# Kernel tuning notes

Measured on AMD Instinct MI355X. Metric: run time of the kernel, lower is better.

The kernel has to match this reference:

```python
import jax, jax.numpy as jnp
import numpy as np

N_NODES = 50000
N_EDGES = 600000
N_GRAPHS = 2048
EMB = 128
N_LAYERS = 3
ATOM_FEATS, ATOM_VOCAB = 9, 100
BOND_FEATS, BOND_VOCAB, BOND_DIM = 3, 8, 3


def setup_inputs() -> dict:
    key = jax.random.key(0)
    ks = jax.random.split(key, 10)
    x = jax.random.randint(ks[0], (N_NODES, ATOM_FEATS), 0, ATOM_VOCAB)
    edge_index = jax.random.randint(ks[1], (2, N_EDGES), 0, N_NODES)
    edge_attr = jax.random.randint(ks[2], (N_EDGES, BOND_FEATS), 0, BOND_VOCAB)
    batch = jnp.sort(jax.random.randint(ks[3], (N_NODES,), 0, N_GRAPHS))
    s = 1.0 / np.sqrt(EMB).astype(np.float32)
    atom_emb = jax.random.normal(ks[4], (ATOM_FEATS, ATOM_VOCAB, EMB), jnp.float32) * 0.1
    bond_emb = jax.random.normal(ks[5], (N_LAYERS, BOND_FEATS, BOND_VOCAB, BOND_DIM), jnp.float32) * 0.1
    W = jax.random.normal(ks[6], (N_LAYERS, BOND_DIM, EMB, EMB), jnp.float32) * s
    b = jnp.zeros((N_LAYERS, BOND_DIM, EMB), jnp.float32)
    fc1_w = jax.random.normal(ks[7], (EMB, EMB), jnp.float32) * s
    fc1_b = jnp.zeros((EMB,), jnp.float32)
    fc2_w = jax.random.normal(ks[8], (EMB, 1), jnp.float32) * s
    fc2_b = jnp.zeros((1,), jnp.float32)
    return dict(x=x, edge_index=edge_index, edge_attr=edge_attr, batch=batch,
                atom_emb=atom_emb, bond_emb=bond_emb, W=W, b=b,
                fc1_w=fc1_w, fc1_b=fc1_b, fc2_w=fc2_w, fc2_b=fc2_b)


def reference(x, edge_index, edge_attr, batch, atom_emb, bond_emb, W, b,
              fc1_w, fc1_b, fc2_w, fc2_b):
    src, dst = edge_index[0], edge_index[1]
    n = x.shape[0]
    # AtomEncoder: sum of per-column embedding lookups -> [N, EMB]
    h = atom_emb[0][x[:, 0]]
    for c in range(1, ATOM_FEATS):
        h = h + atom_emb[c][x[:, c]]
    for layer in range(N_LAYERS):
        # BondEncoder: [E, BOND_DIM] edge weights (one scalar channel per conv)
        ew = bond_emb[layer, 0][edge_attr[:, 0]]
        for c in range(1, BOND_FEATS):
            ew = ew + bond_emb[layer, c][edge_attr[:, c]]
        # Three parallel GCNConv(normalize=False): linear, gather src, edge-weight, scatter-add to dst
        msg = jnp.zeros((edge_index.shape[1], EMB), h.dtype)
        for k in range(BOND_DIM):
            xw = h @ W[layer, k]              # [N, EMB]
            msg = msg + ew[:, k:k + 1] * xw[src]   # [E, EMB]
        agg = jax.ops.segment_sum(msg, dst, num_segments=n)
        hn = agg + jnp.sum(b[layer], axis=0)  # sum of the three conv biases
        if layer < N_LAYERS - 1:
            hn = jax.nn.relu(hn)              # dropout is identity at eval
        h = hn + h                            # residual
    # global_mean_pool
    sums = jax.ops.segment_sum(h, batch, num_segments=N_GRAPHS)
    counts = jax.ops.segment_sum(jnp.ones((n,), h.dtype), batch, num_segments=N_GRAPHS)
    hg = sums / jnp.maximum(counts, 1.0)[:, None]
    return (hg @ fc1_w + fc1_b) @ fc2_w + fc2_b   # [N_GRAPHS, 1]
```

## Files before the change

kernel.cpp:

```cpp
#include <hip/hip_runtime.h>

#define N_NODES 50000
#define N_EDGES 600000
#define N_GRAPHS 2048
#define EMB 128
#define TDIM 384
#define TS_LD 392
#define HN (N_NODES * EMB)
#define GROWS 64

#define EPB 2048
#define NBLKA ((N_EDGES + EPB - 1) / EPB)
#define NCOARSE ((N_NODES + 255) / 256)

#define PRE_ATOM_NB 8334
#define PRE_WCONV_NB 384
#define PRE_GB_NB 131

typedef __attribute__((ext_vector_type(8))) short bf16x8;
typedef __attribute__((ext_vector_type(4))) float f32x4;
#define MFMA_BF16(a, b, c) __builtin_amdgcn_mfma_f32_16x16x32_bf16(a, b, c, 0, 0, 0)

#define AS1 __attribute__((address_space(1)))
#define AS3 __attribute__((address_space(3)))
__device__ inline void gl_lds16(const void* g, void* l) {
  __builtin_amdgcn_global_load_lds((const AS1 void*)g, (AS3 void*)l, 16, 0, 0);
}

__device__ inline unsigned short f2bf(float f) {
  unsigned int u = __float_as_uint(f);
  u += 0x7fffu + ((u >> 16) & 1u);
  return (unsigned short)(u >> 16);
}
__device__ inline float bf2f(unsigned short b) {
  return __uint_as_float(((unsigned int)b) << 16);
}
__device__ inline bf16x8 pack8(float4 lo, float4 hi) {
  bf16x8 r;
  r[0] = (short)f2bf(lo.x); r[1] = (short)f2bf(lo.y);
  r[2] = (short)f2bf(lo.z); r[3] = (short)f2bf(lo.w);
  r[4] = (short)f2bf(hi.x); r[5] = (short)f2bf(hi.y);
  r[6] = (short)f2bf(hi.z); r[7] = (short)f2bf(hi.w);
  return r;
}

__global__ __launch_bounds__(384) void k_pre(const int* __restrict__ x,
                                             const float* __restrict__ atom_emb,
                                             unsigned short* __restrict__ h_bf,
                                             const float* __restrict__ W,
                                             unsigned short* __restrict__ wt,
                                             const int* __restrict__ batch,
                                             int* __restrict__ gs) {
  __shared__ float sb[6 * 1280];
  int blk = blockIdx.x;
  if (blk < PRE_ATOM_NB) {
    const int wv = threadIdx.x >> 6;
    const int lane = threadIdx.x & 63;
    int n = blk * 6 + wv;
    if (n < N_NODES) {
      const int nu = __builtin_amdgcn_readfirstlane(n);
      const int* xr = x + nu * 9;
      int ix[9];
#pragma unroll
      for (int c = 0; c < 9; ++c) ix[c] = xr[c];
      float* wbase = sb + wv * 1280;
      const int half = lane >> 5;
      const int sub16 = lane & 31;
#pragma unroll
      for (int j = 0; j < 4; ++j) {
        int c = 2 * j + half;
        const float* g = atom_emb + (size_t)(c * 100 + ix[c]) * EMB + sub16 * 4;
        gl_lds16(g, wbase + j * 256);
      }
      {
        const float* g = atom_emb + (size_t)(8 * 100 + ix[8]) * EMB + sub16 * 4;
        gl_lds16(g, wbase + 1024);
      }
      asm volatile("s_waitcnt vmcnt(0)" ::: "memory");
      float2 acc = {0.f, 0.f};
#pragma unroll
      for (int c = 0; c < 9; ++c) {
        float2 v = *(const float2*)(wbase + c * 128 + lane * 2);
        acc.x += v.x; acc.y += v.y;
      }
      *(ushort2*)(h_bf + (size_t)nu * EMB + lane * 2) = ushort2{f2bf(acc.x), f2bf(acc.y)};
    }
    return;
  }
  blk -= PRE_ATOM_NB;
  if (blk < PRE_WCONV_NB) {
    int layer = blk >> 7, c = blk & 127, k = threadIdx.x;
    float v = W[(((layer * 3 + (k >> 7)) * 128) + (k & 127)) * 128 + c];
    wt[(size_t)blk * 384 + k] = f2bf(v);
    return;
  }
  blk -= PRE_WCONV_NB;
  {
    int i = blk * 384 + threadIdx.x;
    if (i < N_NODES) {
      int b = batch[i];
      int bp = (i == 0) ? -1 : batch[i - 1];
      for (int g = bp + 1; g <= b; ++g) gs[g] = i;
      if (i == N_NODES - 1) {
        for (int g = b + 1; g <= N_GRAPHS; ++g) gs[g] = N_NODES;
      }
    }
  }
}

__global__ __launch_bounds__(256) void k_cnt(const int* __restrict__ ei,
                                             int* __restrict__ ghist) {
  __shared__ int h[256];
  const int t = threadIdx.x;
  h[t] = 0;
  __syncthreads();
  const int base = blockIdx.x * EPB;
#pragma unroll
  for (int k = 0; k < 8; ++k) {
    int e = base + k * 256 + t;
    if (e < N_EDGES) atomicAdd(&h[ei[N_EDGES + e] >> 8], 1);
  }
  __syncthreads();
  if (t < NCOARSE) ghist[(size_t)t * NBLKA + blockIdx.x] = h[t];
}

__global__ __launch_bounds__(256) void k_sscan(int* __restrict__ ghist,
                                               int* __restrict__ bucket_base,
                                               int* __restrict__ row_start) {
  __shared__ int s[256];
  const int t = threadIdx.x;
  int sum = 0;
  if (t < NCOARSE) {
    int* row = ghist + (size_t)t * NBLKA;
    for (int b = 0; b < NBLKA; ++b) { int v = row[b]; row[b] = sum; sum += v; }
  }
  s[t] = sum;
  __syncthreads();
  for (int off = 1; off < 256; off <<= 1) {
    int v = (t >= off) ? s[t - off] : 0;
    __syncthreads();
    s[t] += v;
    __syncthreads();
  }
  if (t < NCOARSE) bucket_base[t] = s[t] - sum;
  if (t == 0) { bucket_base[NCOARSE] = N_EDGES; row_start[N_NODES] = N_EDGES; }
}

__global__ __launch_bounds__(256) void k_coarse(const int* __restrict__ ei,
                                                const int* __restrict__ ea,
                                                const int* __restrict__ ghist,
                                                const int* __restrict__ bucket_base,
                                                int2* __restrict__ tmp) {
  __shared__ int cnt[256];
  const int t = threadIdx.x;
  cnt[t] = 0;
  __syncthreads();
  const int base = blockIdx.x * EPB;
#pragma unroll
  for (int k = 0; k < 8; ++k) {
    int e = base + k * 256 + t;
    if (e < N_EDGES) {
      int dst = ei[N_EDGES + e];
      int d = dst >> 8;
      int r = atomicAdd(&cnt[d], 1);
      int pos = bucket_base[d] + ghist[(size_t)d * NBLKA + blockIdx.x] + r;
      int eap = ea[e * 3 + 0] | (ea[e * 3 + 1] << 3) | (ea[e * 3 + 2] << 6);
      tmp[pos] = int2{dst | (eap << 16), ei[e]};
    }
  }
}

__global__ __launch_bounds__(256) void k_fine(const int2* __restrict__ tmp,
                                              const int* __restrict__ bucket_base,
                                              int* __restrict__ row_start,
                                              int2* __restrict__ sorted_se) {
  __shared__ int h[256];
  __shared__ int s[256];
  __shared__ int ex[256];
  const int t = threadIdx.x;
  const int d = blockIdx.x;
  const int b0 = bucket_base[d], b1 = bucket_base[d + 1];
  h[t] = 0;
  __syncthreads();
  for (int i = b0 + t; i < b1; i += 256) atomicAdd(&h[tmp[i].x & 255], 1);
  __syncthreads();
  s[t] = h[t];
  __syncthreads();
  for (int off = 1; off < 256; off <<= 1) {
    int v = (t >= off) ? s[t - off] : 0;
    __syncthreads();
    s[t] += v;
    __syncthreads();
  }
  ex[t] = s[t] - h[t];
  int node = d * 256 + t;
  if (node < N_NODES) row_start[node] = b0 + ex[t];
  h[t] = 0;
  __syncthreads();
  for (int i = b0 + t; i < b1; i += 256) {
    int2 r = tmp[i];
    int f = r.x & 255;
    int pos = b0 + ex[f] + atomicAdd(&h[f], 1);
    sorted_se[pos] = int2{r.y, (r.x >> 16) & 511};
  }
}

__global__ __launch_bounds__(256) void k_agg(const int2* __restrict__ sorted_se,
                                             const int* __restrict__ row_start,
                                             const float* __restrict__ bl,
                                             const unsigned short* __restrict__ h_bf,
                                             unsigned short* __restrict__ t_bf) {
  __shared__ float4 combo[512];
  for (int c = threadIdx.x; c < 512; c += 256) {
    int a0 = c & 7, a1 = (c >> 3) & 7, a2 = (c >> 6) & 7;
    combo[c] = float4{bl[a0 * 3 + 0] + bl[24 + a1 * 3 + 0] + bl[48 + a2 * 3 + 0],
                      bl[a0 * 3 + 1] + bl[24 + a1 * 3 + 1] + bl[48 + a2 * 3 + 1],
                      bl[a0 * 3 + 2] + bl[24 + a1 * 3 + 2] + bl[48 + a2 * 3 + 2], 0.f};
  }
  __syncthreads();
  const int node = blockIdx.x * 16 + (threadIdx.x >> 4);
  const int sub = threadIdx.x & 15;
  const int beg = row_start[node], end = row_start[node + 1];
  float4 l0 = {0.f, 0.f, 0.f, 0.f}, h0 = l0;
  float4 l1 = l0, h1 = l0;
  float4 l2 = l0, h2 = l0;
  int e = beg;
  const int full_end = beg + ((end - beg) & ~7);
  for (; e < full_end; e += 8) {
    int2 se[8];
#pragma unroll
    for (int j = 0; j < 8; ++j) se[j] = sorted_se[e + j];
    bf16x8 u[8];
#pragma unroll
    for (int j = 0; j < 8; ++j)
      u[j] = *(const bf16x8*)(h_bf + (size_t)se[j].x * EMB + sub * 8);
#pragma unroll
    for (int j = 0; j < 8; ++j) {
      float4 w = combo[se[j].y];
      float4 vlo = {bf2f((unsigned short)u[j][0]), bf2f((unsigned short)u[j][1]),
                    bf2f((unsigned short)u[j][2]), bf2f((unsigned short)u[j][3])};
      float4 vhi = {bf2f((unsigned short)u[j][4]), bf2f((unsigned short)u[j][5]),
                    bf2f((unsigned short)u[j][6]), bf2f((unsigned short)u[j][7])};
      l0 += vlo * w.x; h0 += vhi * w.x;
      l1 += vlo * w.y; h1 += vhi * w.y;
      l2 += vlo * w.z; h2 += vhi * w.z;
    }
  }
  if (e < end) {
    int2 se[8];
#pragma unroll
    for (int j = 0; j < 8; ++j) {
      int idx = e + j;
      se[j] = sorted_se[idx < end ? idx : end - 1];
    }
    bf16x8 u[8];
#pragma unroll
    for (int j = 0; j < 8; ++j)
      u[j] = *(const bf16x8*)(h_bf + (size_t)se[j].x * EMB + sub * 8);
#pragma unroll
    for (int j = 0; j < 8; ++j) {
      float4 w = (e + j < end) ? combo[se[j].y] : float4{0.f, 0.f, 0.f, 0.f};
      float4 vlo = {bf2f((unsigned short)u[j][0]), bf2f((unsigned short)u[j][1]),
                    bf2f((unsigned short)u[j][2]), bf2f((unsigned short)u[j][3])};
      float4 vhi = {bf2f((unsigned short)u[j][4]), bf2f((unsigned short)u[j][5]),
                    bf2f((unsigned short)u[j][6]), bf2f((unsigned short)u[j][7])};
      l0 += vlo * w.x; h0 += vhi * w.x;
      l1 += vlo * w.y; h1 += vhi * w.y;
      l2 += vlo * w.z; h2 += vhi * w.z;
    }
  }
  size_t base = (size_t)node * TDIM + sub * 8;
  *(bf16x8*)(t_bf + base)       = pack8(l0, h0);
  *(bf16x8*)(t_bf + base + 128) = pack8(l1, h1);
  *(bf16x8*)(t_bf + base + 256) = pack8(l2, h2);
}

__global__ __launch_bounds__(512) void k_gemm(const unsigned short* __restrict__ t_bf,
                                              const unsigned short* __restrict__ wt,
                                              const float* __restrict__ bl,
                                              const unsigned short* __restrict__ h_in_bf,
                                              unsigned short* __restrict__ h_out_bf,
                                              int do_relu) {
  __shared__ unsigned short ts[GROWS * TS_LD];
  const int nb = blockIdx.x * GROWS;
  for (int i = threadIdx.x; i < GROWS * 48; i += 512) {
    int r = i / 48, cc = i % 48;
    bf16x8 v = {};
    int row = nb + r;
    if (row < N_NODES) v = *(const bf16x8*)(t_bf + (size_t)row * TDIM + cc * 8);
    *(bf16x8*)(ts + r * TS_LD + cc * 8) = v;
  }
  __syncthreads();

  const int wv = threadIdx.x >> 6;
  const int lane = threadIdx.x & 63;
  const int m = lane & 15;
  const int kq = lane >> 4;
  const int c = wv * 16 + m;

  const unsigned short* pB = wt + (size_t)c * TDIM + kq * 8;
  bf16x8 B[12];
#pragma unroll
  for (int kc = 0; kc < 12; ++kc) B[kc] = *(const bf16x8*)(pB + kc * 32);

  const float bias = bl[c] + bl[128 + c] + bl[256 + c];

#pragma unroll
  for (int rt = 0; rt < 4; ++rt) {
    const unsigned short* pA = ts + (rt * 16 + m) * TS_LD + kq * 8;
    bf16x8 A[12];
#pragma unroll
    for (int kc = 0; kc < 12; ++kc) A[kc] = *(const bf16x8*)(pA + kc * 32);
    f32x4 acc = {0.f, 0.f, 0.f, 0.f};
#pragma unroll
    for (int kc = 0; kc < 12; ++kc) acc = MFMA_BF16(A[kc], B[kc], acc);
#pragma unroll
    for (int r = 0; r < 4; ++r) {
      int row = nb + rt * 16 + kq * 4 + r;
      if (row < N_NODES) {
        size_t idx = (size_t)row * EMB + c;
        float v = acc[r] + bias;
        if (do_relu) v = fmaxf(v, 0.f);
        float hn = bf2f(h_in_bf[idx]) + v;
        h_out_bf[idx] = f2bf(hn);
      }
    }
  }
}

__global__ __launch_bounds__(128) void k_head(const unsigned short* __restrict__ h_bf,
                                              const int* __restrict__ gs,
                                              const float* __restrict__ fc1_w,
                                              const float* __restrict__ fc1_b,
                                              const float* __restrict__ fc2_w,
                                              const float* __restrict__ fc2_b,
                                              float* __restrict__ out) {
  __shared__ float hg[EMB];
  __shared__ float red[EMB];
  int g = blockIdx.x, e = threadIdx.x;
  int ns = gs[g], ne = gs[g + 1];
  float acc = 0.f;
  for (int n = ns; n < ne; ++n) acc += bf2f(h_bf[(size_t)n * EMB + e]);
  float cnt = fmaxf((float)(ne - ns), 1.f);
  hg[e] = acc / cnt;
  __syncthreads();
  float a2 = fc1_b[e];
  for (int j = 0; j < EMB; ++j) a2 += hg[j] * fc1_w[j * EMB + e];
  red[e] = a2 * fc2_w[e];
  __syncthreads();
  for (int s = 64; s > 0; s >>= 1) {
    if (e < s) red[e] += red[e + s];
    __syncthreads();
  }
  if (e == 0) out[g] = red[0] + fc2_b[0];
}

extern "C" void kernel_launch(void* const* d_in, const int* in_sizes, int n_in,
                              void* d_out, int out_size, void* d_ws, size_t ws_size,
                              hipStream_t stream) {
  const int*   x        = (const int*)d_in[0];
  const int*   ei       = (const int*)d_in[1];
  const int*   ea       = (const int*)d_in[2];
  const int*   batch    = (const int*)d_in[3];
  const float* atom_emb = (const float*)d_in[4];
  const float* bond_emb = (const float*)d_in[5];
  const float* W        = (const float*)d_in[6];
  const float* b        = (const float*)d_in[7];
  const float* fc1_w    = (const float*)d_in[8];
  const float* fc1_b    = (const float*)d_in[9];
  const float* fc2_w    = (const float*)d_in[10];
  const float* fc2_b    = (const float*)d_in[11];
  float* out = (float*)d_out;

  char* p = (char*)d_ws;
  auto alloc = [&](size_t bytes) { char* r = p; p += (bytes + 255) & ~(size_t)255; return r; };
  unsigned short* h0_bf      = (unsigned short*)alloc((size_t)HN * 2);
  unsigned short* h1_bf      = (unsigned short*)alloc((size_t)HN * 2);
  unsigned short* t_bf       = (unsigned short*)alloc((size_t)N_NODES * TDIM * 2);
  unsigned short* wt         = (unsigned short*)alloc((size_t)3 * 128 * TDIM * 2);
  int*            gs         = (int*)alloc((size_t)(N_GRAPHS + 1) * 4);
  int*            row_start  = (int*)alloc((size_t)(N_NODES + 1) * 4);
  int*            ghist      = (int*)alloc((size_t)NCOARSE * NBLKA * 4);
  int*            bucket_base= (int*)alloc((size_t)(NCOARSE + 1) * 4);
  int2*           tmp_se     = (int2*)alloc((size_t)N_EDGES * 8);
  int2*           sorted_se  = (int2*)alloc((size_t)(N_EDGES + 8) * 8);

  const int pre_blocks = PRE_ATOM_NB + PRE_WCONV_NB + PRE_GB_NB;
  k_pre<<<pre_blocks, 384, 0, stream>>>(x, atom_emb, h0_bf, W, wt, batch, gs);
  k_cnt<<<NBLKA, 256, 0, stream>>>(ei, ghist);
  k_sscan<<<1, 256, 0, stream>>>(ghist, bucket_base, row_start);
  k_coarse<<<NBLKA, 256, 0, stream>>>(ei, ea, ghist, bucket_base, tmp_se);
  k_fine<<<NCOARSE, 256, 0, stream>>>(tmp_se, bucket_base, row_start, sorted_se);

  unsigned short* hib = h0_bf;
  unsigned short* hob = h1_bf;
  const int gemm_blocks = (N_NODES + GROWS - 1) / GROWS;
  for (int layer = 0; layer < 3; ++layer) {
    k_agg<<<N_NODES / 16, 256, 0, stream>>>(sorted_se, row_start, bond_emb + layer * 72,
                                            hib, t_bf);
    k_gemm<<<gemm_blocks, 512, 0, stream>>>(
        t_bf, wt + (size_t)layer * 128 * TDIM, b + layer * 3 * EMB,
        hib, hob, layer < 2 ? 1 : 0);
    unsigned short* tb = hib; hib = hob; hob = tb;
  }

  k_head<<<N_GRAPHS, 128, 0, stream>>>(hib, gs, fc1_w, fc1_b, fc2_w, fc2_b, out);
}
```

Measured before the change: 358.3 us.

## Replace single-block serial histogram scan with three-pass multi-block global scan

The old single-block scan had each of 196 threads serially walk its row of 293 histogram entries, with strided global memory access, and then did a small block scan. The new version flattens the bucket-major histogram into one exclusive scan spread across many blocks: block-local scans, a one-block scan of the block partials, and an add-back pass that also writes the bucket bases. k_coarse then reads absolute offsets directly. This adds two kernel launches in exchange for removing the long serial, uncoalesced loop.

```diff
diff --git a/kernel.cpp b/kernel.cpp
--- a/kernel.cpp
+++ b/kernel.cpp
@@ -12,6 +12,8 @@
 #define EPB 2048
 #define NBLKA ((N_EDGES + EPB - 1) / EPB)
 #define NCOARSE ((N_NODES + 255) / 256)
+#define SCAN_TOT (NCOARSE * NBLKA)
+#define SC2_NB ((SCAN_TOT + 255) / 256)
 
 #define PRE_ATOM_NB 8334
 #define PRE_WCONV_NB 384
@@ -124,32 +126,57 @@
   if (t < NCOARSE) ghist[(size_t)t * NBLKA + blockIdx.x] = h[t];
 }
 
-__global__ __launch_bounds__(256) void k_sscan(int* __restrict__ ghist,
-                                               int* __restrict__ bucket_base,
-                                               int* __restrict__ row_start) {
+__global__ __launch_bounds__(256) void k_gscan_a(int* __restrict__ ghist,
+                                                 int* __restrict__ partials) {
   __shared__ int s[256];
   const int t = threadIdx.x;
-  int sum = 0;
-  if (t < NCOARSE) {
-    int* row = ghist + (size_t)t * NBLKA;
-    for (int b = 0; b < NBLKA; ++b) { int v = row[b]; row[b] = sum; sum += v; }
-  }
-  s[t] = sum;
+  const int i = blockIdx.x * 256 + t;
+  int v = (i < SCAN_TOT) ? ghist[i] : 0;
+  s[t] = v;
   __syncthreads();
   for (int off = 1; off < 256; off <<= 1) {
-    int v = (t >= off) ? s[t - off] : 0;
-    __syncthreads();
-    s[t] += v;
-    __syncthreads();
-  }
-  if (t < NCOARSE) bucket_base[t] = s[t] - sum;
+    int u = (t >= off) ? s[t - off] : 0;
+    __syncthreads();
+    s[t] += u;
+    __syncthreads();
+  }
+  if (i < SCAN_TOT) ghist[i] = s[t] - v;
+  if (t == 255) partials[blockIdx.x] = s[255];
+}
+
+__global__ __launch_bounds__(256) void k_gscan_b(int* __restrict__ partials,
+                                                 int* __restrict__ bucket_base,
+                                                 int* __restrict__ row_start) {
+  __shared__ int s[256];
+  const int t = threadIdx.x;
+  int v = (t < SC2_NB) ? partials[t] : 0;
+  s[t] = v;
+  __syncthreads();
+  for (int off = 1; off < 256; off <<= 1) {
+    int u = (t >= off) ? s[t - off] : 0;
+    __syncthreads();
+    s[t] += u;
+    __syncthreads();
+  }
+  if (t < SC2_NB) partials[t] = s[t] - v;
   if (t == 0) { bucket_base[NCOARSE] = N_EDGES; row_start[N_NODES] = N_EDGES; }
+}
+
+__global__ __launch_bounds__(256) void k_gscan_c(int* __restrict__ ghist,
+                                                 const int* __restrict__ partials,
+                                                 int* __restrict__ bucket_base) {
+  const int i = blockIdx.x * 256 + threadIdx.x;
+  if (i < SCAN_TOT) {
+    int g = ghist[i] + partials[blockIdx.x];
+    ghist[i] = g;
+    int d = i / NBLKA;
+    if (i - d * NBLKA == 0) bucket_base[d] = g;
+  }
 }
 
 __global__ __launch_bounds__(256) void k_coarse(const int* __restrict__ ei,
                                                 const int* __restrict__ ea,
                                                 const int* __restrict__ ghist,
-                                                const int* __restrict__ bucket_base,
                                                 int2* __restrict__ tmp) {
   __shared__ int cnt[256];
   const int t = threadIdx.x;
@@ -163,7 +190,7 @@
       int dst = ei[N_EDGES + e];
       int d = dst >> 8;
       int r = atomicAdd(&cnt[d], 1);
-      int pos = bucket_base[d] + ghist[(size_t)d * NBLKA + blockIdx.x] + r;
+      int pos = ghist[(size_t)d * NBLKA + blockIdx.x] + r;
       int eap = ea[e * 3 + 0] | (ea[e * 3 + 1] << 3) | (ea[e * 3 + 2] << 6);
       tmp[pos] = int2{dst | (eap << 16), ei[e]};
     }
@@ -380,7 +407,8 @@
   unsigned short* wt         = (unsigned short*)alloc((size_t)3 * 128 * TDIM * 2);
   int*            gs         = (int*)alloc((size_t)(N_GRAPHS + 1) * 4);
   int*            row_start  = (int*)alloc((size_t)(N_NODES + 1) * 4);
-  int*            ghist      = (int*)alloc((size_t)NCOARSE * NBLKA * 4);
+  int*            ghist      = (int*)alloc((size_t)SCAN_TOT * 4);
+  int*            spart      = (int*)alloc((size_t)SC2_NB * 4);
   int*            bucket_base= (int*)alloc((size_t)(NCOARSE + 1) * 4);
   int2*           tmp_se     = (int2*)alloc((size_t)N_EDGES * 8);
   int2*           sorted_se  = (int2*)alloc((size_t)(N_EDGES + 8) * 8);
@@ -388,8 +416,10 @@
   const int pre_blocks = PRE_ATOM_NB + PRE_WCONV_NB + PRE_GB_NB;
   k_pre<<<pre_blocks, 384, 0, stream>>>(x, atom_emb, h0_bf, W, wt, batch, gs);
   k_cnt<<<NBLKA, 256, 0, stream>>>(ei, ghist);
-  k_sscan<<<1, 256, 0, stream>>>(ghist, bucket_base, row_start);
-  k_coarse<<<NBLKA, 256, 0, stream>>>(ei, ea, ghist, bucket_base, tmp_se);
+  k_gscan_a<<<SC2_NB, 256, 0, stream>>>(ghist, spart);
+  k_gscan_b<<<1, 256, 0, stream>>>(spart, bucket_base, row_start);
+  k_gscan_c<<<SC2_NB, 256, 0, stream>>>(ghist, spart, bucket_base);
+  k_coarse<<<NBLKA, 256, 0, stream>>>(ei, ea, ghist, tmp_se);
   k_fine<<<NCOARSE, 256, 0, stream>>>(tmp_se, bucket_base, row_start, sorted_se);
 
   unsigned short* hib = h0_bf;
```

Result: faster. 320.5 us (-10.5%).
